# Kernel tuning notes

Measured on AMD Instinct MI355X. Metric: run time of the kernel, lower is better.

## Reference

```python
import jax, jax.numpy as jnp
import numpy as np

V, P, C, M, P_ORIG, T = 81920, 131072, 512, 1024, 163840, 262144


def setup_inputs() -> dict:
    key = jax.random.key(0)
    ks = jax.random.split(key, 6)
    adapter_feat = jax.random.normal(ks[0], (V, C), dtype=jnp.float32)
    ce = jax.random.normal(ks[1], (M, C), dtype=jnp.float32)
    # caption embeddings arrive pre-normalized in the original pipeline
    caption_embed = ce / jnp.clip(jnp.linalg.norm(ce, axis=-1, keepdims=True), 1e-12)
    logit_scale = jnp.full((1,), np.log(1.0 / 0.07), dtype=jnp.float32)  # learnable param init
    v2p_map = jax.random.randint(ks[2], (P,), 0, V, dtype=jnp.int32)
    origin_idx = jax.random.randint(ks[3], (P,), 0, P_ORIG, dtype=jnp.int32)
    caption_to_point_mapping = jax.random.randint(ks[4], (T,), 0, P_ORIG, dtype=jnp.int32)
    caption_seg_idx = jnp.sort(jax.random.randint(ks[5], (T,), 0, M, dtype=jnp.int32))
    return {
        "adapter_feat": adapter_feat,
        "caption_embed": caption_embed,
        "logit_scale": logit_scale,
        "v2p_map": v2p_map,
        "origin_idx": origin_idx,
        "caption_to_point_mapping": caption_to_point_mapping,
        "caption_seg_idx": caption_seg_idx,
        "n_origin_points": P_ORIG,
    }


def reference(adapter_feat, caption_embed, logit_scale, v2p_map, origin_idx,
              caption_to_point_mapping, caption_seg_idx, n_origin_points):
    n_pts = v2p_map.shape[0]
    n_captions = caption_embed.shape[0]

    # gather voxel features to points, L2-normalize (feat_norm=True)
    feats = adapter_feat[v2p_map]                                       # [P, C]
    feats = feats / jnp.clip(jnp.linalg.norm(feats, axis=-1, keepdims=True), 1e-12)

    # per-point log-softmax caption scores
    logits = (feats @ caption_embed.T) * jnp.exp(logit_scale[0])        # [P, M]
    scores = jax.nn.log_softmax(logits, axis=-1)                        # [P, M]

    # origin-point -> current-point mapping; -1 where origin point was dropped
    ptom = jnp.full((n_origin_points,), -1, dtype=jnp.int32)
    ptom = ptom.at[origin_idx].set(jnp.arange(n_pts, dtype=jnp.int32))

    gidx = ptom[caption_to_point_mapping]                               # [T]
    invalid = (gidx < 0).astype(scores.dtype)                           # [T]
    # torch negative advanced indexing wraps; replicate faithfully
    safe = jnp.where(gidx < 0, gidx + n_pts, gidx)
    gathered = scores[safe]                                             # [T, M]

    # scatter-sum scores and counts per caption segment
    pooled = jax.ops.segment_sum(gathered, caption_seg_idx, num_segments=n_captions)
    cnt = jax.ops.segment_sum(jnp.ones_like(invalid), caption_seg_idx, num_segments=n_captions)
    ninv = jax.ops.segment_sum(invalid, caption_seg_idx, num_segments=n_captions)
    real_n_points = cnt - ninv                                          # [N]

    denom = jnp.where(real_n_points > 0,
                      1.0 / jnp.where(real_n_points > 0, real_n_points, 1.0), 0.0)
    pooled = pooled * denom[:, None]                                    # [N, M]
    if_has_pts = real_n_points > 0
    return pooled, real_n_points, if_has_pts
```

## Files before the change

### kernel.cpp

```cpp
#include <hip/hip_runtime.h>

#define P_PTS 131072
#define CDIM  512
#define MCAP  1024
#define TLEN  262144
#define PORIG 163840

typedef unsigned short u16;
typedef unsigned char  u8;
typedef __attribute__((ext_vector_type(8))) short short8;
typedef __attribute__((ext_vector_type(4))) float f32x4;
typedef __attribute__((ext_vector_type(8))) int int8v;
typedef __attribute__((ext_vector_type(4))) int int4v;

__device__ __forceinline__ u16 f2bf(float f) {
    unsigned u = __float_as_uint(f);
    unsigned r = (u + 0x7FFFu + ((u >> 16) & 1u)) >> 16;
    return (u16)r;
}
__device__ __forceinline__ float d_e4m3(unsigned x) {
    float f = __uint_as_float((x & 0x7Fu) << 20) * 0x1p120f;
    return __uint_as_float(__float_as_uint(f) | ((x & 0x80u) << 24));
}
__device__ __forceinline__ void ld16(const void* g, void* l) {
    __builtin_amdgcn_global_load_lds(
        (const __attribute__((address_space(1))) void*)g,
        (__attribute__((address_space(3))) void*)l, 16, 0, 0);
}

__global__ __launch_bounds__(256) void cast_cap(const float* __restrict__ cap,
                                                u16* __restrict__ capb,
                                                u8* __restrict__ cap8) {
    int i = (blockIdx.x * 256 + threadIdx.x) * 4;
    float4 v = *(const float4*)(cap + i);
    u16* o = capb + i;
    o[0] = f2bf(v.x); o[1] = f2bf(v.y); o[2] = f2bf(v.z); o[3] = f2bf(v.w);
    int p = __builtin_amdgcn_cvt_pk_fp8_f32(v.x, v.y, 0, false);
    p = __builtin_amdgcn_cvt_pk_fp8_f32(v.z, v.w, p, true);
    *(int*)(cap8 + i) = p;
}

__global__ __launch_bounds__(256) void gather_normalize(
    const float* __restrict__ adapter, const int* __restrict__ v2p,
    u8* __restrict__ feats8) {
    int p = blockIdx.x * 4 + (threadIdx.x >> 6);
    int lane = threadIdx.x & 63;
    int vrow = v2p[p];
    const float4* src = (const float4*)(adapter + (size_t)vrow * CDIM);
    float4 x0 = src[lane * 2];
    float4 x1 = src[lane * 2 + 1];
    float ss = x0.x*x0.x + x0.y*x0.y + x0.z*x0.z + x0.w*x0.w
             + x1.x*x1.x + x1.y*x1.y + x1.z*x1.z + x1.w*x1.w;
    #pragma unroll
    for (int off = 32; off >= 1; off >>= 1) ss += __shfl_xor(ss, off, 64);
    float inv = 1.0f / fmaxf(sqrtf(ss), 1e-12f);
    int lo = __builtin_amdgcn_cvt_pk_fp8_f32(x0.x*inv, x0.y*inv, 0, false);
    lo = __builtin_amdgcn_cvt_pk_fp8_f32(x0.z*inv, x0.w*inv, lo, true);
    int hi = __builtin_amdgcn_cvt_pk_fp8_f32(x1.x*inv, x1.y*inv, 0, false);
    hi = __builtin_amdgcn_cvt_pk_fp8_f32(x1.z*inv, x1.w*inv, hi, true);
    uint2 w; w.x = (unsigned)lo; w.y = (unsigned)hi;
    *(uint2*)(feats8 + (size_t)p * CDIM + lane * 8) = w;
}

__global__ __launch_bounds__(256) void scatter_ptom(const int* __restrict__ oidx,
                                                    int* __restrict__ ptom) {
    int i = blockIdx.x * 256 + threadIdx.x;
    atomicMax(&ptom[oidx[i]], i);
}

__global__ __launch_bounds__(256) void lse_gemm(
    const u8* __restrict__ feats8, const u8* __restrict__ cap8,
    const float* __restrict__ lsc, float* __restrict__ lse_sum) {
    __shared__ __align__(16) u8 As[16384];
    __shared__ __align__(16) u8 Bs[16384];
    const int tid  = threadIdx.x;
    const int wave = tid >> 6;
    const int lane = tid & 63;
    const unsigned id = blockIdx.x;
    const int col0 = (int)((id >> 3) & 7u) * 128;
    const int row0 = (int)((id & 7u) + 8u * (id >> 6)) * 128;
    const int wm = (wave >> 1) * 64;
    const int wn = (wave & 1) * 64;
    const float sf = __expf(lsc[0]);

    f32x4 acc[4][4] = {};

    const int srow = tid >> 3;
    const int kc   = (tid & 7) ^ (srow & 7);
    const u8* gA = feats8 + (size_t)(row0 + srow) * CDIM + kc * 16;
    const u8* gB = cap8   + (size_t)(col0 + srow) * CDIM + kc * 16;
    u8* lA = As + wave * 1024;
    u8* lB = Bs + wave * 1024;

    const int m = lane & 15;
    const int q = lane >> 4;
    const u8* rA1 = As + (size_t)((wm + m) * 8 + ((2*q)   ^ (m & 7))) * 16;
    const u8* rA2 = As + (size_t)((wm + m) * 8 + ((2*q+1) ^ (m & 7))) * 16;
    const u8* rB1 = Bs + (size_t)((wn + m) * 8 + ((2*q)   ^ (m & 7))) * 16;
    const u8* rB2 = Bs + (size_t)((wn + m) * 8 + ((2*q+1) ^ (m & 7))) * 16;

    for (int k0 = 0; k0 < CDIM; k0 += 128) {
        __syncthreads();
        #pragma unroll
        for (int c = 0; c < 4; ++c) {
            ld16(gA + (size_t)c * 32 * CDIM + k0, lA + c * 4096);
            ld16(gB + (size_t)c * 32 * CDIM + k0, lB + c * 4096);
        }
        __syncthreads();
        int8v af[4], bv[4];
        #pragma unroll
        for (int i = 0; i < 4; ++i) {
            int4v lo = *(const int4v*)(rA1 + i * 2048);
            int4v hi = *(const int4v*)(rA2 + i * 2048);
            af[i][0]=lo[0]; af[i][1]=lo[1]; af[i][2]=lo[2]; af[i][3]=lo[3];
            af[i][4]=hi[0]; af[i][5]=hi[1]; af[i][6]=hi[2]; af[i][7]=hi[3];
        }
        #pragma unroll
        for (int j = 0; j < 4; ++j) {
            int4v lo = *(const int4v*)(rB1 + j * 2048);
            int4v hi = *(const int4v*)(rB2 + j * 2048);
            bv[j][0]=lo[0]; bv[j][1]=lo[1]; bv[j][2]=lo[2]; bv[j][3]=lo[3];
            bv[j][4]=hi[0]; bv[j][5]=hi[1]; bv[j][6]=hi[2]; bv[j][7]=hi[3];
        }
        #pragma unroll
        for (int i = 0; i < 4; ++i)
            #pragma unroll
            for (int j = 0; j < 4; ++j)
                acc[i][j] = __builtin_amdgcn_mfma_scale_f32_16x16x128_f8f6f4(
                    af[i], bv[j], acc[i][j], 0, 0, 0, 127,
                    0, 127);
    }

    #pragma unroll
    for (int i = 0; i < 4; ++i) {
        float s4[4] = {0.f, 0.f, 0.f, 0.f};
        #pragma unroll
        for (int j = 0; j < 4; ++j)
            #pragma unroll
            for (int r = 0; r < 4; ++r)
                s4[r] += __expf(acc[i][j][r] * sf - sf);
        #pragma unroll
        for (int off = 8; off >= 1; off >>= 1)
            #pragma unroll
            for (int r = 0; r < 4; ++r)
                s4[r] += __shfl_xor(s4[r], off, 64);
        if (m == 0) {
            int rbase = row0 + wm + i * 16 + q * 4;
            #pragma unroll
            for (int r = 0; r < 4; ++r)
                atomicAdd(&lse_sum[rbase + r], s4[r]);
        }
    }
}

__device__ __forceinline__ int lower_bound(const int* __restrict__ a, int n, int key) {
    int lo = 0, hi = n;
    while (lo < hi) { int mid = (lo + hi) >> 1; if (a[mid] < key) lo = mid + 1; else hi = mid; }
    return lo;
}

__global__ __launch_bounds__(1024) void seg_reduce(
    const u8* __restrict__ feats8, const float* __restrict__ lse_sum,
    const int* __restrict__ ptom, const int* __restrict__ ctpm,
    const int* __restrict__ seg, const float* __restrict__ lsc,
    u16* __restrict__ Fb, float* __restrict__ Lout, float* __restrict__ realn) {
    int s = blockIdx.x;
    int tid = threadIdx.x, wave = tid >> 6, lane = tid & 63;
    int start = lower_bound(seg, TLEN, s);
    int end   = lower_bound(seg, TLEN, s + 1);
    float a[8] = {0,0,0,0,0,0,0,0};
    float Lacc = 0.f; int inv = 0;
    for (int r = start + wave; r < end; r += 16) {
        int g = ptom[ctpm[r]];
        int row = (g < 0) ? g + P_PTS : g;
        if (lane == 0) { inv += (g < 0); Lacc += __logf(lse_sum[row]); }
        uint2 v = *(const uint2*)(feats8 + (size_t)row * CDIM + lane * 8);
        a[0] += d_e4m3(v.x);       a[1] += d_e4m3(v.x >> 8);
        a[2] += d_e4m3(v.x >> 16); a[3] += d_e4m3(v.x >> 24);
        a[4] += d_e4m3(v.y);       a[5] += d_e4m3(v.y >> 8);
        a[6] += d_e4m3(v.y >> 16); a[7] += d_e4m3(v.y >> 24);
    }
    __shared__ float pF[16][512];
    __shared__ float pL[16];
    __shared__ int   pI[16];
    #pragma unroll
    for (int u = 0; u < 8; ++u) pF[wave][lane * 8 + u] = a[u];
    if (lane == 0) { pL[wave] = Lacc; pI[wave] = inv; }
    __syncthreads();
    if (tid < 512) {
        float f = 0.f;
        #pragma unroll
        for (int w = 0; w < 16; ++w) f += pF[w][tid];
        Fb[(size_t)s * CDIM + tid] = f2bf(f);
    }
    if (tid == 0) {
        float cnt = (float)(end - start);
        float Ls = 0.f; int ninv = 0;
        #pragma unroll
        for (int w = 0; w < 16; ++w) { Ls += pL[w]; ninv += pI[w]; }
        realn[s] = cnt - (float)ninv;
        Lout[s] = Ls + __expf(lsc[0]) * cnt;
    }
}

__global__ __launch_bounds__(256) void pooled_gemm(
    const u16* __restrict__ Fb, const u16* __restrict__ capb,
    const float* __restrict__ Lout, const float* __restrict__ realn,
    const float* __restrict__ lsc, float* __restrict__ out) {
    __shared__ __align__(16) u16 As[128 * 32];
    __shared__ __align__(16) u16 Bs[128 * 32];
    const int tid  = threadIdx.x;
    const int wave = tid >> 6;
    const int lane = tid & 63;
    const int col0 = blockIdx.x * 128;
    const int row0 = blockIdx.y * 128;
    const int wm = (wave >> 1) * 64;
    const int wn = (wave & 1) * 64;
    const float sf = __expf(lsc[0]);
    f32x4 acc[4][4] = {};
    const int srow = tid >> 2;
    const int scol = (tid & 3) * 8;
    const u16* gA0 = Fb   + (size_t)(row0 + srow) * CDIM + scol;
    const u16* gB0 = capb + (size_t)(col0 + srow) * CDIM + scol;
    u16* lA0 = As + wave * 512;
    u16* lB0 = Bs + wave * 512;
    const int mrow = lane & 15;
    const int quad = lane >> 4;
    const u16* rA = As + (wm + mrow) * 32 + quad * 8;
    const u16* rB = Bs + (wn + mrow) * 32 + quad * 8;
    for (int k0 = 0; k0 < CDIM; k0 += 32) {
        __syncthreads();
        ld16(gA0 + k0,             lA0);
        ld16(gA0 + 64 * CDIM + k0, lA0 + 2048);
        ld16(gB0 + k0,             lB0);
        ld16(gB0 + 64 * CDIM + k0, lB0 + 2048);
        __syncthreads();
        short8 af[4], bfr[4];
        #pragma unroll
        for (int i = 0; i < 4; ++i) af[i]  = *(const short8*)(rA + i * 512);
        #pragma unroll
        for (int j = 0; j < 4; ++j) bfr[j] = *(const short8*)(rB + j * 512);
        #pragma unroll
        for (int i = 0; i < 4; ++i)
            #pragma unroll
            for (int j = 0; j < 4; ++j)
                acc[i][j] = __builtin_amdgcn_mfma_f32_16x16x32_bf16(
                    af[i], bfr[j], acc[i][j], 0, 0, 0);
    }
    #pragma unroll
    for (int i = 0; i < 4; ++i) {
        #pragma unroll
        for (int r = 0; r < 4; ++r) {
            int s = row0 + wm + i * 16 + quad * 4 + r;
            float rn = realn[s];
            float dn = rn > 0.f ? 1.0f / rn : 0.0f;
            float L = Lout[s];
            #pragma unroll
            for (int j = 0; j < 4; ++j) {
                int mc = col0 + wn + j * 16 + mrow;
                out[(size_t)s * MCAP + mc] = (sf * acc[i][j][r] - L) * dn;
            }
        }
    }
}

__global__ __launch_bounds__(256) void write_tail(const float* __restrict__ realn,
                                                  float* __restrict__ out) {
    int s = blockIdx.x * 256 + threadIdx.x;
    if (s < MCAP) {
        float r = realn[s];
        out[MCAP * MCAP + s] = r;
        out[MCAP * MCAP + MCAP + s] = (r > 0.f) ? 1.0f : 0.0f;
    }
}

extern "C" void kernel_launch(void* const* d_in, const int* in_sizes, int n_in,
                              void* d_out, int out_size, void* d_ws, size_t ws_size,
                              hipStream_t stream) {
    const float* adapter = (const float*)d_in[0];
    const float* cap     = (const float*)d_in[1];
    const float* lsc     = (const float*)d_in[2];
    const int*   v2p     = (const int*)d_in[3];
    const int*   oidx    = (const int*)d_in[4];
    const int*   ctpm    = (const int*)d_in[5];
    const int*   seg     = (const int*)d_in[6];
    float* out = (float*)d_out;

    char* ws = (char*)d_ws;
    u8*    feats8  = (u8*)(ws);
    u8*    cap8    = (u8*)(ws + 67108864);
    u16*   capb    = (u16*)(ws + 67633152);
    float* lse_sum = (float*)(ws + 68681728);
    int*   ptom    = (int*)(ws + 69206016);
    u16*   Fb      = (u16*)(ws + 69861376);
    float* Lout    = (float*)(ws + 70909952);
    float* realn   = (float*)(ws + 70914048);

    hipMemsetAsync(ptom, 0xFF, (size_t)PORIG * 4, stream);
    hipMemsetAsync(lse_sum, 0, (size_t)P_PTS * 4, stream);

    cast_cap<<<(MCAP * CDIM) / 1024, 256, 0, stream>>>(cap, capb, cap8);
    gather_normalize<<<P_PTS / 4, 256, 0, stream>>>(adapter, v2p, feats8);
    scatter_ptom<<<P_PTS / 256, 256, 0, stream>>>(oidx, ptom);
    lse_gemm<<<(P_PTS / 128) * (MCAP / 128), 256, 0, stream>>>(feats8, cap8, lsc, lse_sum);
    seg_reduce<<<MCAP, 1024, 0, stream>>>(feats8, lse_sum, ptom, ctpm, seg, lsc, Fb, Lout, realn);
    pooled_gemm<<<dim3(MCAP / 128, MCAP / 128), 256, 0, stream>>>(Fb, capb, Lout, realn, lsc, out);
    write_tail<<<4, 256, 0, stream>>>(realn, out);
}
```

Baseline: 442.9 us.

## Merge small prep kernels, precompute gather rows, shrink pooled GEMM tiles

The caption cast, the ptom scatter and the lse_sum zeroing are merged into one prep kernel, which drops a memset and a launch. A new make_rows kernel resolves the ptom[ctpm] double indirection ahead of time into packed row indices with an invalid bit, and seg_reduce is unrolled by two to expose more memory-level parallelism. The pooled GEMM tile goes from 128 to 64 so more blocks cover the 1024x1024 output, and write_tail is folded into it. These are several small launch-overhead and latency tweaks, at the cost of an extra pass over the T-length index array.

```diff
diff --git a/kernel.cpp b/kernel.cpp
--- a/kernel.cpp
+++ b/kernel.cpp
@@ -28,16 +28,27 @@
         (__attribute__((address_space(3))) void*)l, 16, 0, 0);
 }
 
-__global__ __launch_bounds__(256) void cast_cap(const float* __restrict__ cap,
-                                                u16* __restrict__ capb,
-                                                u8* __restrict__ cap8) {
-    int i = (blockIdx.x * 256 + threadIdx.x) * 4;
-    float4 v = *(const float4*)(cap + i);
-    u16* o = capb + i;
-    o[0] = f2bf(v.x); o[1] = f2bf(v.y); o[2] = f2bf(v.z); o[3] = f2bf(v.w);
-    int p = __builtin_amdgcn_cvt_pk_fp8_f32(v.x, v.y, 0, false);
-    p = __builtin_amdgcn_cvt_pk_fp8_f32(v.z, v.w, p, true);
-    *(int*)(cap8 + i) = p;
+__global__ __launch_bounds__(256) void prep(const float* __restrict__ cap,
+                                            const int* __restrict__ oidx,
+                                            u16* __restrict__ capb,
+                                            u8* __restrict__ cap8,
+                                            int* __restrict__ ptom,
+                                            float* __restrict__ lse_sum) {
+    int b = blockIdx.x, tid = threadIdx.x;
+    if (b < 512) {
+        int i = (b * 256 + tid) * 4;
+        float4 v = *(const float4*)(cap + i);
+        u16* o = capb + i;
+        o[0] = f2bf(v.x); o[1] = f2bf(v.y); o[2] = f2bf(v.z); o[3] = f2bf(v.w);
+        int p = __builtin_amdgcn_cvt_pk_fp8_f32(v.x, v.y, 0, false);
+        p = __builtin_amdgcn_cvt_pk_fp8_f32(v.z, v.w, p, true);
+        *(int*)(cap8 + i) = p;
+        int t = b * 256 + tid;
+        atomicMax(&ptom[oidx[t]], t);
+    } else {
+        int j = (b - 512) * 256 + tid;
+        lse_sum[j] = 0.0f;
+    }
 }
 
 __global__ __launch_bounds__(256) void gather_normalize(
@@ -62,10 +73,12 @@
     *(uint2*)(feats8 + (size_t)p * CDIM + lane * 8) = w;
 }
 
-__global__ __launch_bounds__(256) void scatter_ptom(const int* __restrict__ oidx,
-                                                    int* __restrict__ ptom) {
-    int i = blockIdx.x * 256 + threadIdx.x;
-    atomicMax(&ptom[oidx[i]], i);
+__global__ __launch_bounds__(256) void make_rows(const int* __restrict__ ctpm,
+                                                 const int* __restrict__ ptom,
+                                                 unsigned* __restrict__ rows) {
+    int t = blockIdx.x * 256 + threadIdx.x;
+    int g = ptom[ctpm[t]];
+    rows[t] = (g < 0) ? ((unsigned)(g + P_PTS) | 0x80000000u) : (unsigned)g;
 }
 
 __global__ __launch_bounds__(256) void lse_gemm(
@@ -99,6 +112,7 @@
     const u8* rB1 = Bs + (size_t)((wn + m) * 8 + ((2*q)   ^ (m & 7))) * 16;
     const u8* rB2 = Bs + (size_t)((wn + m) * 8 + ((2*q+1) ^ (m & 7))) * 16;
 
+    #pragma unroll
     for (int k0 = 0; k0 < CDIM; k0 += 128) {
         __syncthreads();
         #pragma unroll
@@ -127,8 +141,7 @@
             #pragma unroll
             for (int j = 0; j < 4; ++j)
                 acc[i][j] = __builtin_amdgcn_mfma_scale_f32_16x16x128_f8f6f4(
-                    af[i], bv[j], acc[i][j], 0, 0, 0, 127,
-                    0, 127);
+                    af[i], bv[j], acc[i][j], 0, 0, 0, 127, 0, 127);
     }
 
     #pragma unroll
@@ -161,8 +174,8 @@
 
 __global__ __launch_bounds__(1024) void seg_reduce(
     const u8* __restrict__ feats8, const float* __restrict__ lse_sum,
-    const int* __restrict__ ptom, const int* __restrict__ ctpm,
-    const int* __restrict__ seg, const float* __restrict__ lsc,
+    const unsigned* __restrict__ rows, const int* __restrict__ seg,
+    const float* __restrict__ lsc,
     u16* __restrict__ Fb, float* __restrict__ Lout, float* __restrict__ realn) {
     int s = blockIdx.x;
     int tid = threadIdx.x, wave = tid >> 6, lane = tid & 63;
@@ -170,15 +183,34 @@
     int end   = lower_bound(seg, TLEN, s + 1);
     float a[8] = {0,0,0,0,0,0,0,0};
     float Lacc = 0.f; int inv = 0;
-    for (int r = start + wave; r < end; r += 16) {
-        int g = ptom[ctpm[r]];
-        int row = (g < 0) ? g + P_PTS : g;
-        if (lane == 0) { inv += (g < 0); Lacc += __logf(lse_sum[row]); }
-        uint2 v = *(const uint2*)(feats8 + (size_t)row * CDIM + lane * 8);
-        a[0] += d_e4m3(v.x);       a[1] += d_e4m3(v.x >> 8);
-        a[2] += d_e4m3(v.x >> 16); a[3] += d_e4m3(v.x >> 24);
-        a[4] += d_e4m3(v.y);       a[5] += d_e4m3(v.y >> 8);
-        a[6] += d_e4m3(v.y >> 16); a[7] += d_e4m3(v.y >> 24);
+    int r = start + wave;
+    for (; r + 16 < end; r += 32) {
+        unsigned p0 = rows[r], p1 = rows[r + 16];
+        int r0 = (int)(p0 & 0x7FFFFFFFu), r1 = (int)(p1 & 0x7FFFFFFFu);
+        uint2 v0 = *(const uint2*)(feats8 + (size_t)r0 * CDIM + lane * 8);
+        uint2 v1 = *(const uint2*)(feats8 + (size_t)r1 * CDIM + lane * 8);
+        if (lane == 0) {
+            inv += (int)(p0 >> 31) + (int)(p1 >> 31);
+            Lacc += __logf(lse_sum[r0]) + __logf(lse_sum[r1]);
+        }
+        a[0] += d_e4m3(v0.x);       a[1] += d_e4m3(v0.x >> 8);
+        a[2] += d_e4m3(v0.x >> 16); a[3] += d_e4m3(v0.x >> 24);
+        a[4] += d_e4m3(v0.y);       a[5] += d_e4m3(v0.y >> 8);
+        a[6] += d_e4m3(v0.y >> 16); a[7] += d_e4m3(v0.y >> 24);
+        a[0] += d_e4m3(v1.x);       a[1] += d_e4m3(v1.x >> 8);
+        a[2] += d_e4m3(v1.x >> 16); a[3] += d_e4m3(v1.x >> 24);
+        a[4] += d_e4m3(v1.y);       a[5] += d_e4m3(v1.y >> 8);
+        a[6] += d_e4m3(v1.y >> 16); a[7] += d_e4m3(v1.y >> 24);
+    }
+    if (r < end) {
+        unsigned p0 = rows[r];
+        int r0 = (int)(p0 & 0x7FFFFFFFu);
+        uint2 v0 = *(const uint2*)(feats8 + (size_t)r0 * CDIM + lane * 8);
+        if (lane == 0) { inv += (int)(p0 >> 31); Lacc += __logf(lse_sum[r0]); }
+        a[0] += d_e4m3(v0.x);       a[1] += d_e4m3(v0.x >> 8);
+        a[2] += d_e4m3(v0.x >> 16); a[3] += d_e4m3(v0.x >> 24);
+        a[4] += d_e4m3(v0.y);       a[5] += d_e4m3(v0.y >> 8);
+        a[6] += d_e4m3(v0.y >> 16); a[7] += d_e4m3(v0.y >> 24);
     }
     __shared__ float pF[16][512];
     __shared__ float pL[16];
@@ -207,17 +239,17 @@
     const u16* __restrict__ Fb, const u16* __restrict__ capb,
     const float* __restrict__ Lout, const float* __restrict__ realn,
     const float* __restrict__ lsc, float* __restrict__ out) {
-    __shared__ __align__(16) u16 As[128 * 32];
-    __shared__ __align__(16) u16 Bs[128 * 32];
+    __shared__ __align__(16) u16 As[64 * 32];
+    __shared__ __align__(16) u16 Bs[64 * 32];
     const int tid  = threadIdx.x;
     const int wave = tid >> 6;
     const int lane = tid & 63;
-    const int col0 = blockIdx.x * 128;
-    const int row0 = blockIdx.y * 128;
-    const int wm = (wave >> 1) * 64;
-    const int wn = (wave & 1) * 64;
+    const int col0 = blockIdx.x * 64;
+    const int row0 = blockIdx.y * 64;
+    const int wm = (wave >> 1) * 32;
+    const int wn = (wave & 1) * 32;
     const float sf = __expf(lsc[0]);
-    f32x4 acc[4][4] = {};
+    f32x4 acc[2][2] = {};
     const int srow = tid >> 2;
     const int scol = (tid & 3) * 8;
     const u16* gA0 = Fb   + (size_t)(row0 + srow) * CDIM + scol;
@@ -228,27 +260,26 @@
     const int quad = lane >> 4;
     const u16* rA = As + (wm + mrow) * 32 + quad * 8;
     const u16* rB = Bs + (wn + mrow) * 32 + quad * 8;
+    #pragma unroll 4
     for (int k0 = 0; k0 < CDIM; k0 += 32) {
         __syncthreads();
-        ld16(gA0 + k0,             lA0);
-        ld16(gA0 + 64 * CDIM + k0, lA0 + 2048);
-        ld16(gB0 + k0,             lB0);
-        ld16(gB0 + 64 * CDIM + k0, lB0 + 2048);
+        ld16(gA0 + k0, lA0);
+        ld16(gB0 + k0, lB0);
         __syncthreads();
-        short8 af[4], bfr[4];
-        #pragma unroll
-        for (int i = 0; i < 4; ++i) af[i]  = *(const short8*)(rA + i * 512);
-        #pragma unroll
-        for (int j = 0; j < 4; ++j) bfr[j] = *(const short8*)(rB + j * 512);
-        #pragma unroll
-        for (int i = 0; i < 4; ++i)
-            #pragma unroll
-            for (int j = 0; j < 4; ++j)
+        short8 af[2], bfr[2];
+        #pragma unroll
+        for (int i = 0; i < 2; ++i) af[i]  = *(const short8*)(rA + i * 512);
+        #pragma unroll
+        for (int j = 0; j < 2; ++j) bfr[j] = *(const short8*)(rB + j * 512);
+        #pragma unroll
+        for (int i = 0; i < 2; ++i)
+            #pragma unroll
+            for (int j = 0; j < 2; ++j)
                 acc[i][j] = __builtin_amdgcn_mfma_f32_16x16x32_bf16(
                     af[i], bfr[j], acc[i][j], 0, 0, 0);
     }
     #pragma unroll
-    for (int i = 0; i < 4; ++i) {
+    for (int i = 0; i < 2; ++i) {
         #pragma unroll
         for (int r = 0; r < 4; ++r) {
             int s = row0 + wm + i * 16 + quad * 4 + r;
@@ -256,21 +287,17 @@
             float dn = rn > 0.f ? 1.0f / rn : 0.0f;
             float L = Lout[s];
             #pragma unroll
-            for (int j = 0; j < 4; ++j) {
+            for (int j = 0; j < 2; ++j) {
                 int mc = col0 + wn + j * 16 + mrow;
                 out[(size_t)s * MCAP + mc] = (sf * acc[i][j][r] - L) * dn;
             }
         }
     }
-}
-
-__global__ __launch_bounds__(256) void write_tail(const float* __restrict__ realn,
-                                                  float* __restrict__ out) {
-    int s = blockIdx.x * 256 + threadIdx.x;
-    if (s < MCAP) {
-        float r = realn[s];
-        out[MCAP * MCAP + s] = r;
-        out[MCAP * MCAP + MCAP + s] = (r > 0.f) ? 1.0f : 0.0f;
+    if (col0 == 0 && tid < 64) {
+        int s = row0 + tid;
+        float rv = realn[s];
+        out[MCAP * MCAP + s] = rv;
+        out[MCAP * MCAP + MCAP + s] = (rv > 0.f) ? 1.0f : 0.0f;
     }
 }
 
@@ -287,23 +314,22 @@
     float* out = (float*)d_out;
 
     char* ws = (char*)d_ws;
-    u8*    feats8  = (u8*)(ws);
-    u8*    cap8    = (u8*)(ws + 67108864);
-    u16*   capb    = (u16*)(ws + 67633152);
-    float* lse_sum = (float*)(ws + 68681728);
-    int*   ptom    = (int*)(ws + 69206016);
-    u16*   Fb      = (u16*)(ws + 69861376);
-    float* Lout    = (float*)(ws + 70909952);
-    float* realn   = (float*)(ws + 70914048);
+    u8*       feats8  = (u8*)(ws);
+    u8*       cap8    = (u8*)(ws + 67108864);
+    u16*      capb    = (u16*)(ws + 67633152);
+    float*    lse_sum = (float*)(ws + 68681728);
+    int*      ptom    = (int*)(ws + 69206016);
+    unsigned* rows    = (unsigned*)(ws + 69861376);
+    u16*      Fb      = (u16*)(ws + 70909952);
+    float*    Lout    = (float*)(ws + 71958528);
+    float*    realn   = (float*)(ws + 71962624);
 
     hipMemsetAsync(ptom, 0xFF, (size_t)PORIG * 4, stream);
-    hipMemsetAsync(lse_sum, 0, (size_t)P_PTS * 4, stream);
-
-    cast_cap<<<(MCAP * CDIM) / 1024, 256, 0, stream>>>(cap, capb, cap8);
+
+    prep<<<1024, 256, 0, stream>>>(cap, oidx, capb, cap8, ptom, lse_sum);
     gather_normalize<<<P_PTS / 4, 256, 0, stream>>>(adapter, v2p, feats8);
-    scatter_ptom<<<P_PTS / 256, 256, 0, stream>>>(oidx, ptom);
+    make_rows<<<TLEN / 256, 256, 0, stream>>>(ctpm, ptom, rows);
     lse_gemm<<<(P_PTS / 128) * (MCAP / 128), 256, 0, stream>>>(feats8, cap8, lsc, lse_sum);
-    seg_reduce<<<MCAP, 1024, 0, stream>>>(feats8, lse_sum, ptom, ctpm, seg, lsc, Fb, Lout, realn);
-    pooled_gemm<<<dim3(MCAP / 128, MCAP / 128), 256, 0, stream>>>(Fb, capb, Lout, realn, lsc, out);
-    write_tail<<<4, 256, 0, stream>>>(realn, out);
-}
+    seg_reduce<<<MCAP, 1024, 0, stream>>>(feats8, lse_sum, rows, seg, lsc, Fb, Lout, realn);
+    pooled_gemm<<<dim3(MCAP / 64, MCAP / 64), 256, 0, stream>>>(Fb, capb, Lout, realn, lsc, out);
+}
```

New measurement: 410.2 us. -7.4%, faster.
